# Performance work log

Measured on AMD Instinct MI355X. Metric: run time of the kernel, lower is better.

## Reference

```python
import jax, jax.numpy as jnp
import numpy as np
from jax import lax

B, NCH, T = 256, 32, 2000
NTF, NSF, NSUB, TK = 4, 40, 20, 25
NCLS = 4
NTAN = NSUB * (NSUB + 1) // 2
REIG_EPS = 1e-4


def setup_inputs() -> dict:
    key = jax.random.key(0)
    ks = jax.random.split(key, 8)
    x = jax.random.normal(ks[0], (B, NCH, T), dtype=jnp.float32)
    conv1_w = jax.random.normal(ks[1], (NTF, 1, 1, TK), dtype=jnp.float32) * 0.2
    conv1_b = jnp.zeros((NTF,), dtype=jnp.float32)
    conv2_w = jax.random.normal(ks[2], (NSF, NTF, NCH, 1), dtype=jnp.float32) * 0.1
    conv2_b = jnp.zeros((NSF,), dtype=jnp.float32)
    # BiMap weight: semi-orthogonal (n_subspace x n_spatial_filters) via QR
    A = jax.random.normal(ks[3], (NSF, NSUB), dtype=jnp.float32)
    Q, _ = jnp.linalg.qr(A)
    W_bimap = Q.T  # (NSUB, NSF), rows orthonormal
    clf_w = jax.random.normal(ks[4], (NCLS, NTAN), dtype=jnp.float32) * 0.05
    clf_b = jnp.zeros((NCLS,), dtype=jnp.float32)
    return {"x": x, "conv1_w": conv1_w, "conv1_b": conv1_b,
            "conv2_w": conv2_w, "conv2_b": conv2_b,
            "W_bimap": W_bimap, "clf_w": clf_w, "clf_b": clf_b}


def _forward(x, conv1_w, conv1_b, conv2_w, conv2_b, W_bimap, clf_w, clf_b):
    dn = ('NCHW', 'OIHW', 'NCHW')
    h = x[:, None, :, :]  # (B,1,NCH,T)
    # temporal conv, 'same' with reflect padding along time
    pl = (TK - 1) // 2
    pr = TK - 1 - pl
    hp = jnp.pad(h, ((0, 0), (0, 0), (0, 0), (pl, pr)), mode='reflect')
    h1 = lax.conv_general_dilated(hp, conv1_w, (1, 1), 'VALID', dimension_numbers=dn)
    h1 = h1 + conv1_b[None, :, None, None]  # (B,NTF,NCH,T)
    # spatial conv collapses channel axis
    h2 = lax.conv_general_dilated(h1, conv2_w, (1, 1), 'VALID', dimension_numbers=dn)
    h2 = h2 + conv2_b[None, :, None, None]  # (B,NSF,1,T)
    h2 = h2.reshape(B, NSF, T)
    # covariance pooling over time (unbiased)
    hm = h2 - h2.mean(axis=-1, keepdims=True)
    C = jnp.einsum('bft,bgt->bfg', hm, hm) / (T - 1)  # (B,NSF,NSF)
    # BiMap: S = W C W^T  -> (B,NSUB,NSUB)
    S = jnp.einsum('if,bfg,jg->bij', W_bimap, C, W_bimap)
    # ReEig: clamp eigenvalues at threshold
    w, U = jnp.linalg.eigh(S)
    w = jnp.maximum(w, REIG_EPS)
    S = jnp.einsum('bik,bk,bjk->bij', U, w, U)
    # LogEig: matrix log, take scaled upper triangle, flatten
    w2, U2 = jnp.linalg.eigh(S)
    L = jnp.einsum('bik,bk,bjk->bij', U2, jnp.log(w2), U2)
    iu, ju = jnp.triu_indices(NSUB)
    scale = jnp.where(iu == ju, 1.0, jnp.sqrt(2.0)).astype(L.dtype)
    z = L[:, iu, ju] * scale[None, :]  # (B, NTAN)
    return z @ clf_w.T + clf_b


def reference(x, conv1_w, conv1_b, conv2_w, conv2_b, W_bimap, clf_w, clf_b):
    return _forward(x, conv1_w, conv1_b, conv2_w, conv2_b, W_bimap, clf_w, clf_b)
```

## Files before the change

kernel.cpp:

```cpp
#include <hip/hip_runtime.h>
#include <math.h>

#define B_    256
#define NCH   32
#define T_    2000
#define NTF   4
#define NSF   40
#define NSUB  20
#define TK    25
#define NCLS  4
#define NTAN  210
#define NPAIR 820
#define ACC_STRIDE 860
#define TILE_T 250
#define NTILE  8
#define PL     12

#define ACC_FLOATS (B_*ACC_STRIDE)
#define W2T_OFF ACC_FLOATS
#define W1T_OFF (ACC_FLOATS + NSF*NTF*NCH)

#define XS_TSTR 36
#define H2_STR  252
#define LDS_DW  10080

typedef float v2f __attribute__((ext_vector_type(2)));

__device__ __forceinline__ v2f fma2(v2f a, v2f b, v2f c) {
#if __has_builtin(__builtin_elementwise_fma)
    return __builtin_elementwise_fma(a, b, c);
#else
    v2f r; r.x = fmaf(a.x, b.x, c.x); r.y = fmaf(a.y, b.y, c.y); return r;
#endif
}

__device__ __forceinline__ int pack_ut(int f, int g) {
    return f*NSF - (f*(f-1))/2 + (g - f);
}

__global__ void prep_kernel(const float* __restrict__ conv1_w,
                            const float* __restrict__ conv2_w,
                            float* __restrict__ ws) {
    int tid = threadIdx.x;
    float* w2t = ws + W2T_OFF;
    float* w1t = ws + W1T_OFF;
    for (int i = tid; i < NSF*NTF*NCH; i += 256) {
        int f  = i & 3;
        int sc = i >> 2;
        int c  = sc & 31;
        int s  = sc >> 5;
        w2t[i] = conv2_w[(s*NTF + f)*NCH + c];
    }
    for (int i = tid; i < NTF*TK; i += 256) {
        int f = i & 3;
        int k = i >> 2;
        w1t[i] = conv1_w[f*TK + k];
    }
}

__global__ __launch_bounds__(256, 2)
void conv_gram_kernel(const float* __restrict__ x,
                      const float* __restrict__ conv1_b,
                      const float* __restrict__ conv2_b,
                      const float* __restrict__ wts,
                      float* __restrict__ acc)
{
    __shared__ float lds[LDS_DW];

    const int tid  = threadIdx.x;
    const int bid  = blockIdx.x;
    const int b    = bid >> 3;
    const int tile = bid & 7;
    const int t0   = tile * TILE_T;

    const float* xb = x + (size_t)b*NCH*T_;
    for (int li = tid; li < NCH*280; li += 256) {
        int c = li / 280;
        int i = li - c*280;
        int tg = t0 + i - PL;
        tg = (tg < 0) ? -tg : tg;
        tg = (tg >= T_) ? (2*T_ - 2 - tg) : tg;
        lds[i*XS_TSTR + c] = xb[c*T_ + tg];
    }
    __syncthreads();

    const float4* w1t = (const float4*)(wts + W1T_OFF);
    const float4* w2t = (const float4*)(wts + W2T_OFF);

    v2f h1[64];
    {
        float b0 = conv1_b[0], b1 = conv1_b[1], b2 = conv1_b[2], b3 = conv1_b[3];
        #pragma unroll
        for (int c = 0; c < NCH; ++c) {
            v2f lo; lo.x = b0; lo.y = b1;
            v2f hi; hi.x = b2; hi.y = b3;
            h1[2*c]   = lo;
            h1[2*c+1] = hi;
        }
    }
    #pragma clang loop unroll(disable)
    for (int k = 0; k < TK; ++k) {
        float4 wq = w1t[k];
        v2f w01; w01.x = wq.x; w01.y = wq.y;
        v2f w23; w23.x = wq.z; w23.y = wq.w;
        const float4* xr = (const float4*)&lds[(tid + k)*XS_TSTR];
        float4 xv4[8];
        #pragma unroll
        for (int j = 0; j < 8; ++j) xv4[j] = xr[j];
        const float* xv = (const float*)xv4;
        #pragma unroll
        for (int c = 0; c < NCH; ++c) {
            v2f xc; xc.x = xv[c]; xc.y = xv[c];
            h1[2*c]   = fma2(xc, w01, h1[2*c]);
            h1[2*c+1] = fma2(xc, w23, h1[2*c+1]);
        }
    }
    __syncthreads();

    #pragma clang loop unroll_count(2)
    for (int s = 0; s < NSF; ++s) {
        v2f a01; a01.x = conv2_b[s]; a01.y = 0.f;
        v2f a23; a23.x = 0.f;        a23.y = 0.f;
        #pragma unroll
        for (int c = 0; c < NCH; ++c) {
            float4 wq = w2t[s*NCH + c];
            v2f w01; w01.x = wq.x; w01.y = wq.y;
            v2f w23; w23.x = wq.z; w23.y = wq.w;
            a01 = fma2(w01, h1[2*c],   a01);
            a23 = fma2(w23, h1[2*c+1], a23);
        }
        float v = (a01.x + a01.y) + (a23.x + a23.y);
        if (tid < H2_STR) lds[s*H2_STR + tid] = (tid < TILE_T) ? v : 0.f;
    }
    __syncthreads();

    float* accb = acc + b*ACC_STRIDE;

    if (tid < 55) {
        int bf = 0, rem = tid;
        while (rem >= 10 - bf) { rem -= 10 - bf; bf++; }
        int bg = bf + rem;

        const float4* rA[4];
        const float4* rB[4];
        #pragma unroll
        for (int a = 0; a < 4; ++a) {
            rA[a] = (const float4*)&lds[(4*bf + a)*H2_STR];
            rB[a] = (const float4*)&lds[(4*bg + a)*H2_STR];
        }
        v2f accL[16], accH[16];
        #pragma unroll
        for (int i = 0; i < 16; ++i) { accL[i] = (v2f)0.f; accH[i] = (v2f)0.f; }

        #pragma unroll 7
        for (int q = 0; q < H2_STR/4; ++q) {
            float4 av[4], bv[4];
            #pragma unroll
            for (int a = 0; a < 4; ++a) av[a] = rA[a][q];
            #pragma unroll
            for (int a = 0; a < 4; ++a) bv[a] = rB[a][q];
            #pragma unroll
            for (int a = 0; a < 4; ++a) {
                v2f aL; aL.x = av[a].x; aL.y = av[a].y;
                v2f aH; aH.x = av[a].z; aH.y = av[a].w;
                #pragma unroll
                for (int g = 0; g < 4; ++g) {
                    v2f bL; bL.x = bv[g].x; bL.y = bv[g].y;
                    v2f bH; bH.x = bv[g].z; bH.y = bv[g].w;
                    accL[a*4+g] = fma2(aL, bL, accL[a*4+g]);
                    accH[a*4+g] = fma2(aH, bH, accH[a*4+g]);
                }
            }
        }
        #pragma unroll
        for (int a = 0; a < 4; ++a) {
            #pragma unroll
            for (int g = 0; g < 4; ++g) {
                int f  = 4*bf + a;
                int gg = 4*bg + g;
                if (f <= gg) {
                    v2f sL = accL[a*4+g], sH = accH[a*4+g];
                    float s = (sL.x + sL.y) + (sH.x + sH.y);
                    atomicAdd(&accb[pack_ut(f, gg)], s);
                }
            }
        }
    }

    if (tid >= 64 && tid < 64 + NSF) {
        int row = tid - 64;
        const float4* rr = (const float4*)&lds[row*H2_STR];
        float csum = 0.f;
        #pragma unroll 7
        for (int q = 0; q < H2_STR/4; ++q) {
            float4 v = rr[q];
            csum += (v.x + v.y) + (v.z + v.w);
        }
        atomicAdd(&accb[NPAIR + row], csum);
    }
}

__device__ __forceinline__ void pq_sched(int r, int k, int& p, int& q) {
    if (k == 0) { p = 19; q = r; }
    else {
        int a = r + k;      if (a >= 19) a -= 19;
        int d = r - k + 19; if (d >= 19) d -= 19;
        p = a; q = d;
    }
}

__global__ __launch_bounds__(128)
void finalize_kernel(const float* __restrict__ acc,
                     const float* __restrict__ W_bimap,
                     const float* __restrict__ clf_w,
                     const float* __restrict__ clf_b,
                     float* __restrict__ out)
{
    __shared__ float C[NSF*NSF];
    __shared__ float Wb[NSUB*NSF];
    __shared__ float M[NSUB*NSF];
    __shared__ float A[NSUB*21];
    __shared__ float V[NSUB*21];
    __shared__ float cs_c[10], cs_s[10];
    __shared__ float lam[NSUB];
    __shared__ float z[NTAN];

    const int tid = threadIdx.x;
    const int b   = blockIdx.x;
    const float* accb = acc + b*ACC_STRIDE;

    for (int i = tid; i < NSF*NSF; i += 128) {
        int f = i / NSF, g = i % NSF;
        int lo = f < g ? f : g;
        int hi = f < g ? g : f;
        double G  = (double)accb[pack_ut(lo, hi)];
        double sf = (double)accb[NPAIR + f];
        double sg = (double)accb[NPAIR + g];
        C[i] = (float)((G - sf*sg/(double)T_) / (double)(T_ - 1));
    }
    for (int i = tid; i < NSUB*NSF; i += 128) Wb[i] = W_bimap[i];
    __syncthreads();

    for (int i = tid; i < NSUB*NSF; i += 128) {
        int r = i / NSF, g = i % NSF;
        float s = 0.f;
        #pragma unroll 8
        for (int f = 0; f < NSF; ++f) s = fmaf(Wb[r*NSF+f], C[f*NSF+g], s);
        M[i] = s;
    }
    __syncthreads();

    for (int i = tid; i < NSUB*NSUB; i += 128) {
        int r = i / NSUB, j = i % NSUB;
        float s = 0.f;
        #pragma unroll 8
        for (int g = 0; g < NSF; ++g) s = fmaf(M[r*NSF+g], Wb[j*NSF+g], s);
        A[r*21+j] = s;
        V[r*21+j] = (r == j) ? 1.f : 0.f;
    }
    __syncthreads();

    const int kk = tid / 10;
    const int ll = tid - 10*(tid/10);

    for (int sweep = 0; sweep < 7; ++sweep) {
        for (int r = 0; r < 19; ++r) {
            if (tid < 10) {
                int p, q; pq_sched(r, tid, p, q);
                float app = A[p*21+p], aqq = A[q*21+q], apq = A[p*21+q];
                float c = 1.f, s = 0.f;
                if (fabsf(apq) > 1e-30f) {
                    float tau = (aqq - app) / (2.f*apq);
                    float t = 1.f / (fabsf(tau) + sqrtf(1.f + tau*tau));
                    if (tau < 0.f) t = -t;
                    c = 1.f / sqrtf(1.f + t*t);
                    s = t * c;
                }
                cs_c[tid] = c; cs_s[tid] = s;
            }
            __syncthreads();
            if (tid < 100) {
                int pk, qk, pl, ql;
                pq_sched(r, kk, pk, qk);
                pq_sched(r, ll, pl, ql);
                float ck = cs_c[kk], sk = cs_s[kk];
                float cl = cs_c[ll], sl = cs_s[ll];
                float a00 = A[pk*21+pl], a01 = A[pk*21+ql];
                float a10 = A[qk*21+pl], a11 = A[qk*21+ql];
                float t00 = ck*a00 - sk*a10, t01 = ck*a01 - sk*a11;
                float t10 = sk*a00 + ck*a10, t11 = sk*a01 + ck*a11;
                A[pk*21+pl] = cl*t00 - sl*t01;
                A[pk*21+ql] = sl*t00 + cl*t01;
                A[qk*21+pl] = cl*t10 - sl*t11;
                A[qk*21+ql] = sl*t10 + cl*t11;
                float v00 = V[pk*21+pl], v01 = V[pk*21+ql];
                float v10 = V[qk*21+pl], v11 = V[qk*21+ql];
                V[pk*21+pl] = cl*v00 - sl*v01;
                V[pk*21+ql] = sl*v00 + cl*v01;
                V[qk*21+pl] = cl*v10 - sl*v11;
                V[qk*21+ql] = sl*v10 + cl*v11;
            }
            __syncthreads();
        }
    }

    if (tid < NSUB) {
        float w = A[tid*21+tid];
        lam[tid] = logf(fmaxf(w, 1e-4f));
    }
    __syncthreads();

    for (int p = tid; p < NTAN; p += 128) {
        int i = 0, rem = p;
        while (rem >= NSUB - i) { rem -= NSUB - i; i++; }
        int j = i + rem;
        float s = 0.f;
        #pragma unroll 5
        for (int k = 0; k < NSUB; ++k) s = fmaf(V[i*21+k]*lam[k], V[j*21+k], s);
        z[p] = (i == j) ? s : s * 1.41421356237309515f;
    }
    __syncthreads();

    if (tid < NCLS) {
        float s = clf_b[tid];
        for (int p = 0; p < NTAN; ++p) s = fmaf(clf_w[tid*NTAN+p], z[p], s);
        out[b*NCLS + tid] = s;
    }
}

extern "C" void kernel_launch(void* const* d_in, const int* in_sizes, int n_in,
                              void* d_out, int out_size, void* d_ws, size_t ws_size,
                              hipStream_t stream) {
    const float* x       = (const float*)d_in[0];
    const float* conv1_w = (const float*)d_in[1];
    const float* conv1_b = (const float*)d_in[2];
    const float* conv2_w = (const float*)d_in[3];
    const float* conv2_b = (const float*)d_in[4];
    const float* W_bimap = (const float*)d_in[5];
    const float* clf_w   = (const float*)d_in[6];
    const float* clf_b   = (const float*)d_in[7];
    float* out = (float*)d_out;
    float* ws  = (float*)d_ws;

    hipMemsetAsync(ws, 0, (size_t)ACC_FLOATS*sizeof(float), stream);

    prep_kernel<<<1, 256, 0, stream>>>(conv1_w, conv2_w, ws);
    conv_gram_kernel<<<B_*NTILE, 256, 0, stream>>>(x, conv1_b, conv2_b, ws, ws);
    finalize_kernel<<<B_, 128, 0, stream>>>(ws, W_bimap, clf_w, clf_b, out);
}
```

Measured before the change: 328.8 us.

## Restructure conv loop per channel to cut register pressure and raise occupancy

The temporal conv is now computed one channel at a time and immediately folded into 40 spatial-filter accumulators, replacing the 64-element per-thread h1 register array. The x tile is stored channel-major in LDS, spatial weights are repacked in pairs, and conv1 bias is folded into a precomputed combined bias. Launch bounds go from 2 to 4 blocks per SM to exploit the lower register use. The trade-off is re-reading the conv1 weights for every channel and more scalar/global weight loads per FMA.

Measured after the change: 422.6 us. 1.29x slower.

```diff
diff --git a/kernel.cpp b/kernel.cpp
--- a/kernel.cpp
+++ b/kernel.cpp
@@ -17,12 +17,13 @@
 #define PL     12
 
 #define ACC_FLOATS (B_*ACC_STRIDE)
-#define W2T_OFF ACC_FLOATS
-#define W1T_OFF (ACC_FLOATS + NSF*NTF*NCH)
-
-#define XS_TSTR 36
-#define H2_STR  252
-#define LDS_DW  10080
+#define W2P_OFF ACC_FLOATS
+#define W1T_OFF (W2P_OFF + NCH*NTF*NSF)
+#define CB_OFF  (W1T_OFF + NTF*TK)
+
+#define XS_STR 284
+#define H2_STR 252
+#define LDS_DW 10080
 
 typedef float v2f __attribute__((ext_vector_type(2)));
 
@@ -39,29 +40,41 @@
 }
 
 __global__ void prep_kernel(const float* __restrict__ conv1_w,
+                            const float* __restrict__ conv1_b,
                             const float* __restrict__ conv2_w,
+                            const float* __restrict__ conv2_b,
                             float* __restrict__ ws) {
     int tid = threadIdx.x;
-    float* w2t = ws + W2T_OFF;
+    float* w2p = ws + W2P_OFF;
     float* w1t = ws + W1T_OFF;
-    for (int i = tid; i < NSF*NTF*NCH; i += 256) {
-        int f  = i & 3;
-        int sc = i >> 2;
-        int c  = sc & 31;
-        int s  = sc >> 5;
-        w2t[i] = conv2_w[(s*NTF + f)*NCH + c];
+    float* cb  = ws + CB_OFF;
+    for (int i = tid; i < NCH*NTF*20; i += 256) {
+        int s2 = i % 20;
+        int cf = i / 20;
+        int f  = cf & 3;
+        int c  = cf >> 2;
+        w2p[2*i]   = conv2_w[((2*s2  )*NTF + f)*NCH + c];
+        w2p[2*i+1] = conv2_w[((2*s2+1)*NTF + f)*NCH + c];
     }
     for (int i = tid; i < NTF*TK; i += 256) {
         int f = i & 3;
         int k = i >> 2;
         w1t[i] = conv1_w[f*TK + k];
     }
-}
-
-__global__ __launch_bounds__(256, 2)
+    if (tid < NSF) {
+        float s = conv2_b[tid];
+        #pragma unroll
+        for (int f = 0; f < NTF; ++f) {
+            float a = 0.f;
+            for (int c = 0; c < NCH; ++c) a += conv2_w[(tid*NTF + f)*NCH + c];
+            s = fmaf(a, conv1_b[f], s);
+        }
+        cb[tid] = s;
+    }
+}
+
+__global__ __launch_bounds__(256, 4)
 void conv_gram_kernel(const float* __restrict__ x,
-                      const float* __restrict__ conv1_b,
-                      const float* __restrict__ conv2_b,
                       const float* __restrict__ wts,
                       float* __restrict__ acc)
 {
@@ -74,63 +87,64 @@
     const int t0   = tile * TILE_T;
 
     const float* xb = x + (size_t)b*NCH*T_;
-    for (int li = tid; li < NCH*280; li += 256) {
-        int c = li / 280;
-        int i = li - c*280;
-        int tg = t0 + i - PL;
-        tg = (tg < 0) ? -tg : tg;
-        tg = (tg >= T_) ? (2*T_ - 2 - tg) : tg;
-        lds[i*XS_TSTR + c] = xb[c*T_ + tg];
+    for (int c = 0; c < NCH; ++c) {
+        for (int i = tid; i < 280; i += 256) {
+            int tg = t0 + i - PL;
+            tg = (tg < 0) ? -tg : tg;
+            tg = (tg >= T_) ? (2*T_ - 2 - tg) : tg;
+            lds[c*XS_STR + i] = xb[c*T_ + tg];
+        }
     }
     __syncthreads();
 
     const float4* w1t = (const float4*)(wts + W1T_OFF);
-    const float4* w2t = (const float4*)(wts + W2T_OFF);
-
-    v2f h1[64];
-    {
-        float b0 = conv1_b[0], b1 = conv1_b[1], b2 = conv1_b[2], b3 = conv1_b[3];
-        #pragma unroll
-        for (int c = 0; c < NCH; ++c) {
-            v2f lo; lo.x = b0; lo.y = b1;
-            v2f hi; hi.x = b2; hi.y = b3;
-            h1[2*c]   = lo;
-            h1[2*c+1] = hi;
-        }
-    }
-    #pragma clang loop unroll(disable)
-    for (int k = 0; k < TK; ++k) {
-        float4 wq = w1t[k];
-        v2f w01; w01.x = wq.x; w01.y = wq.y;
-        v2f w23; w23.x = wq.z; w23.y = wq.w;
-        const float4* xr = (const float4*)&lds[(tid + k)*XS_TSTR];
-        float4 xv4[8];
-        #pragma unroll
-        for (int j = 0; j < 8; ++j) xv4[j] = xr[j];
-        const float* xv = (const float*)xv4;
-        #pragma unroll
-        for (int c = 0; c < NCH; ++c) {
-            v2f xc; xc.x = xv[c]; xc.y = xv[c];
-            h1[2*c]   = fma2(xc, w01, h1[2*c]);
-            h1[2*c+1] = fma2(xc, w23, h1[2*c+1]);
-        }
-    }
-    __syncthreads();
+    const float2* cbp = (const float2*)(wts + CB_OFF);
+    const float2* w2p = (const float2*)(wts + W2P_OFF);
+
+    v2f acc2[20];
+    #pragma unroll
+    for (int s2 = 0; s2 < 20; ++s2) {
+        float2 cbv = cbp[s2];
+        v2f a; a.x = cbv.x; a.y = cbv.y;
+        acc2[s2] = a;
+    }
 
     #pragma clang loop unroll_count(2)
-    for (int s = 0; s < NSF; ++s) {
-        v2f a01; a01.x = conv2_b[s]; a01.y = 0.f;
-        v2f a23; a23.x = 0.f;        a23.y = 0.f;
-        #pragma unroll
-        for (int c = 0; c < NCH; ++c) {
-            float4 wq = w2t[s*NCH + c];
+    for (int c = 0; c < NCH; ++c) {
+        const float* xr = &lds[c*XS_STR + tid];
+        v2f h1a = (v2f)0.f, h1b = (v2f)0.f;
+        #pragma unroll
+        for (int k = 0; k < TK; ++k) {
+            float xv = xr[k];
+            float4 wq = w1t[k];
             v2f w01; w01.x = wq.x; w01.y = wq.y;
             v2f w23; w23.x = wq.z; w23.y = wq.w;
-            a01 = fma2(w01, h1[2*c],   a01);
-            a23 = fma2(w23, h1[2*c+1], a23);
-        }
-        float v = (a01.x + a01.y) + (a23.x + a23.y);
-        if (tid < H2_STR) lds[s*H2_STR + tid] = (tid < TILE_T) ? v : 0.f;
+            v2f xv2; xv2.x = xv;  xv2.y = xv;
+            h1a = fma2(xv2, w01, h1a);
+            h1b = fma2(xv2, w23, h1b);
+        }
+        const float2* wp = w2p + c*(NTF*20);
+        float hf[4] = {h1a.x, h1a.y, h1b.x, h1b.y};
+        #pragma unroll
+        for (int f = 0; f < NTF; ++f) {
+            v2f hb; hb.x = hf[f]; hb.y = hf[f];
+            #pragma unroll
+            for (int s2 = 0; s2 < 20; ++s2) {
+                float2 w = wp[f*20 + s2];
+                v2f wv; wv.x = w.x; wv.y = w.y;
+                acc2[s2] = fma2(hb, wv, acc2[s2]);
+            }
+        }
+    }
+    __syncthreads();
+
+    if (tid < H2_STR) {
+        const bool valid = (tid < TILE_T);
+        #pragma unroll
+        for (int s2 = 0; s2 < 20; ++s2) {
+            lds[(2*s2  )*H2_STR + tid] = valid ? acc2[s2].x : 0.f;
+            lds[(2*s2+1)*H2_STR + tid] = valid ? acc2[s2].y : 0.f;
+        }
     }
     __syncthreads();
 
@@ -344,7 +358,7 @@
 
     hipMemsetAsync(ws, 0, (size_t)ACC_FLOATS*sizeof(float), stream);
 
-    prep_kernel<<<1, 256, 0, stream>>>(conv1_w, conv2_w, ws);
-    conv_gram_kernel<<<B_*NTILE, 256, 0, stream>>>(x, conv1_b, conv2_b, ws, ws);
+    prep_kernel<<<1, 256, 0, stream>>>(conv1_w, conv1_b, conv2_w, conv2_b, ws);
+    conv_gram_kernel<<<B_*NTILE, 256, 0, stream>>>(x, ws, ws);
     finalize_kernel<<<B_, 128, 0, stream>>>(ws, W_bimap, clf_w, clf_b, out);
 }
```
